# Kernel optimization log

Hardware: AMD Instinct MI355X
Metric: run time of the kernel (lower is better)

## Reference

```python
import jax, jax.numpy as jnp
import numpy as np

EMB = 768  # SentenceT5 embedding dim; MLP input is 2*EMB


def setup_inputs() -> dict:
    key = jax.random.key(0)
    ks = jax.random.split(key, 9)
    B, S, D = 32, 32, 64
    num_doc = jax.random.randint(ks[0], (B,), 8, D + 1, dtype=jnp.int32)
    num_doc = num_doc.at[0].set(D)  # ensure max == padded dim (tf.reduce_max semantics)
    num_seg = jax.random.randint(ks[1], (B,), 4, S + 1, dtype=jnp.int32)
    num_seg = num_seg.at[0].set(S)
    doc_emb = jax.random.normal(ks[2], (B, D, EMB), jnp.float32)
    sum_emb = jax.random.normal(ks[3], (B, S, EMB), jnp.float32)
    # ragged .to_tensor() -> zero rows beyond per-sample length
    doc_emb = doc_emb * (jnp.arange(D)[None, :, None] < num_doc[:, None, None])
    sum_emb = sum_emb * (jnp.arange(S)[None, :, None] < num_seg[:, None, None])
    target_agg = jax.random.uniform(ks[4], (B,), jnp.float32)
    target_inst = jax.random.uniform(ks[5], (B, S), jnp.float32)
    w = lambda k, i, o: jax.random.normal(k, (i, o), jnp.float32) * 0.02
    W1 = w(ks[6], 2 * EMB, EMB)
    b1 = jnp.zeros((EMB,), jnp.float32)
    W2 = w(ks[7], EMB, EMB // 2)
    b2 = jnp.zeros((EMB // 2,), jnp.float32)
    W3 = w(ks[8], EMB // 2, 1)
    b3 = jnp.zeros((1,), jnp.float32)
    return dict(doc_emb=doc_emb, sum_emb=sum_emb, num_document_splits=num_doc,
                num_summary_segments=num_seg, target_agg_score=target_agg,
                target_instance_score=target_inst,
                W1=W1, b1=b1, W2=W2, b2=b2, W3=W3, b3=b3)


def _forward(doc_emb, sum_emb, num_doc, num_seg, W1, b1, W2, b2, W3, b3):
    B, D, E = doc_emb.shape
    S = sum_emb.shape[1]
    # concat([doc, seg]) @ W1 == doc @ W1[:E] + seg @ W1[E:]  (avoids materializing [B,S,D,2E])
    h_doc = jnp.einsum('bde,eh->bdh', doc_emb, W1[:E])   # [B,D,E]
    h_seg = jnp.einsum('bse,eh->bsh', sum_emb, W1[E:])   # [B,S,E]
    h1 = jax.nn.gelu(h_doc[:, None, :, :] + h_seg[:, :, None, :] + b1, approximate=False)  # [B,S,D,E]
    h2 = jax.nn.gelu(jnp.einsum('bsdh,hk->bsdk', h1, W2) + b2, approximate=False)          # [B,S,D,E/2]
    score = jax.nn.sigmoid(jnp.einsum('bsdk,ko->bsdo', h2, W3) + b3)[..., 0]               # [B,S,D]
    mask_d = (jnp.arange(D)[None, :] < num_doc[:, None]).astype(jnp.float32)               # [B,D]
    seg_max = jnp.max(mask_d[:, None, :] * score, axis=-1)                                 # [B,S]
    seg_w = jnp.where(num_seg > 10, 1.0, 100.0).astype(jnp.float32)                        # [B]
    pred = seg_w[:, None] * seg_max                                                        # [B,S]
    # cosine similarity prior (keras CosineSimilarity returns -cos)
    dn = doc_emb * jax.lax.rsqrt(jnp.maximum(jnp.sum(doc_emb * doc_emb, -1, keepdims=True), 1e-12))
    sn = sum_emb * jax.lax.rsqrt(jnp.maximum(jnp.sum(sum_emb * sum_emb, -1, keepdims=True), 1e-12))
    cs = -jnp.einsum('bde,bse->bsd', dn, sn)                                               # [B,S,D]
    dscos = jnp.max(mask_d[:, None, :] * (1.0 + cs) * 0.5, axis=-1)                        # [B,S]
    seg_mask = (jnp.arange(S)[None, :] < num_seg[:, None]).astype(jnp.float32)             # [B,S]
    diff = jnp.abs(dscos - pred) * seg_mask
    cos_prior = jnp.mean(jnp.sum(diff, axis=1) / num_seg.astype(jnp.float32))
    return pred, cos_prior


def reference(doc_emb, sum_emb, num_document_splits, num_summary_segments,
              target_agg_score, target_instance_score,
              W1, b1, W2, b2, W3, b3):
    B, S = target_instance_score.shape
    seg_mask = jnp.arange(S)[None, :] < num_summary_segments[:, None]
    # pad target instance scores with ones beyond per-sample length
    target_instance = jnp.where(seg_mask, target_instance_score, 1.0)
    pred, cos_prior = _forward(doc_emb, sum_emb, num_document_splits, num_summary_segments,
                               W1, b1, W2, b2, W3, b3)
    return (target_agg_score, target_instance, pred, num_summary_segments, cos_prior)
```

## Files before the change

### kernel.cpp

```cpp
#include <hip/hip_runtime.h>
#include <hip/hip_bf16.h>
#include <math.h>


typedef __bf16 bf16x8 __attribute__((ext_vector_type(8)));
typedef float f32x4 __attribute__((ext_vector_type(4)));

__device__ __forceinline__ unsigned short f2bf(float x) {
    unsigned int u = __float_as_uint(x);
    u = (u + 0x7fffu + ((u >> 16) & 1u)) >> 16;
    return (unsigned short)u;
}
__device__ __forceinline__ float exp2_fast(float x) {
    float r; asm("v_exp_f32 %0, %1" : "=v"(r) : "v"(x)); return r;
}
__device__ __forceinline__ float rcp_fast(float x) {
    float r; asm("v_rcp_f32 %0, %1" : "=v"(r) : "v"(x)); return r;
}
__device__ __forceinline__ unsigned int cvt_pk_bf16(float lo, float hi) {
    unsigned int r; asm("v_cvt_pk_bf16_f32 %0, %1, %2" : "=v"(r) : "v"(lo), "v"(hi)); return r;
}
__device__ __forceinline__ float gelu_fast(float x) {
    float t = x * fmaf(x * x, -0.10294325f, -2.3022081f);
    return x * rcp_fast(1.0f + exp2_fast(t));
}
__device__ __forceinline__ float sigmoid_fast(float x) {
    return rcp_fast(1.0f + exp2_fast(x * -1.4426950408889634f));
}
__device__ __forceinline__ float wave_sum(float v) {
    for (int o = 32; o; o >>= 1) v += __shfl_xor(v, o);
    return v;
}
__device__ __forceinline__ float wave_max(float v) {
    for (int o = 32; o; o >>= 1) v = fmaxf(v, __shfl_xor(v, o));
    return v;
}
__device__ __forceinline__ void soft_barrier() {
    __builtin_amdgcn_sched_barrier(0);
    asm volatile("s_waitcnt lgkmcnt(0)" ::: "memory");
    __builtin_amdgcn_s_barrier();
    __builtin_amdgcn_sched_barrier(0);
}
#define GLOAD_LDS16(GP, LP)                                                     \
    __builtin_amdgcn_global_load_lds(                                           \
        (const __attribute__((address_space(1))) unsigned int*)(GP),            \
        (__attribute__((address_space(3))) unsigned int*)(LP), 16, 0, 0)

__global__ __launch_bounds__(256) void prep_all(const float* __restrict__ W1,
                                                const float* __restrict__ W2,
                                                const float* __restrict__ doc,
                                                const float* __restrict__ sume,
                                                unsigned short* __restrict__ W1t,
                                                unsigned short* __restrict__ W2f,
                                                unsigned short* __restrict__ dnbf,
                                                unsigned short* __restrict__ snbf) {
    __shared__ __align__(16) char shbuf[49152];
    int id = blockIdx.x;
    int t = threadIdx.x;
    if (id < 288) {
        float (*tile)[65] = (float(*)[65])shbuf;
        int bx = id % 12, by = id / 12;
        int r0 = by * 64, c0 = bx * 64;
        #pragma unroll
        for (int p = 0; p < 16; ++p) {
            int r = p * 4 + (t >> 6), c = t & 63;
            tile[r][c] = W1[(r0 + r) * 768 + c0 + c];
        }
        __syncthreads();
        #pragma unroll
        for (int p = 0; p < 16; ++p) {
            int cc = p * 4 + (t >> 6), rr = t & 63;
            W1t[(c0 + cc) * 1536 + r0 + rr] = f2bf(tile[rr][cc]);
        }
    } else if (id < 300) {
        unsigned short* sh = (unsigned short*)shbuf;
        int kt = id - 288;
        #pragma unroll
        for (int p = 0; p < 96; ++p) {
            int u = p * 256 + t;
            int k = u / 384, n = u - k * 384;
            sh[u] = f2bf(W2[(kt * 64 + k) * 384 + n]);
        }
        __syncthreads();
        #pragma unroll
        for (int p = 0; p < 12; ++p) {
            int u = p * 256 + t;
            int lane = u & 63;
            int g = u >> 6;
            int ks = g / 24, fc = g - ks * 24;
            unsigned short tmp[8];
            #pragma unroll
            for (int j = 0; j < 8; ++j)
                tmp[j] = sh[(ks * 32 + (lane >> 4) * 8 + j) * 384 + fc * 16 + (lane & 15)];
            int ktks = kt * 2 + ks;
            *(uint4*)(W2f + ((ktks * 24 + fc) * 64 + lane) * 8) = *(uint4*)tmp;
        }
    } else {
        int row = (id - 300) * 4 + (t >> 6);
        int lane = t & 63;
        const float* p; unsigned short* dst;
        if (row < 2048) { p = doc + row * 768; dst = dnbf + row * 768; }
        else            { p = sume + (row - 2048) * 768; dst = snbf + (row - 2048) * 768; }
        const float* pp = p + lane * 12;
        float4 a0 = *(const float4*)(pp);
        float4 a1 = *(const float4*)(pp + 4);
        float4 a2 = *(const float4*)(pp + 8);
        float s = a0.x*a0.x + a0.y*a0.y + a0.z*a0.z + a0.w*a0.w
                + a1.x*a1.x + a1.y*a1.y + a1.z*a1.z + a1.w*a1.w
                + a2.x*a2.x + a2.y*a2.y + a2.z*a2.z + a2.w*a2.w;
        s = wave_sum(s);
        float r = rsqrtf(fmaxf(s, 1e-12f));
        unsigned short* dd = dst + lane * 12;
        dd[0]  = f2bf(a0.x * r); dd[1]  = f2bf(a0.y * r);
        dd[2]  = f2bf(a0.z * r); dd[3]  = f2bf(a0.w * r);
        dd[4]  = f2bf(a1.x * r); dd[5]  = f2bf(a1.y * r);
        dd[6]  = f2bf(a1.z * r); dd[7]  = f2bf(a1.w * r);
        dd[8]  = f2bf(a2.x * r); dd[9]  = f2bf(a2.y * r);
        dd[10] = f2bf(a2.z * r); dd[11] = f2bf(a2.w * r);
    }
}

__global__ __launch_bounds__(256) void gemm1(const float* __restrict__ doc,
                                             const float* __restrict__ sume,
                                             const unsigned short* __restrict__ W1t,
                                             const float* __restrict__ b1,
                                             unsigned short* __restrict__ hd,
                                             unsigned short* __restrict__ hs) {
    __shared__ __align__(16) unsigned short Asw[2][128 * 64];
    __shared__ __align__(16) unsigned short Bsw[2][64 * 64];
    int t = threadIdx.x;
    int row0 = blockIdx.y * 128, col0 = blockIdx.x * 64;
    bool is_doc = row0 < 2048;
    const float* A = is_doc ? (doc + row0 * 768) : (sume + (row0 - 2048) * 768);
    int kbase = is_doc ? 0 : 768;
    unsigned short* O = is_doc ? (hd + row0 * 768) : (hs + (row0 - 2048) * 768);

    int l = t & 63, w = t >> 6;
    int wr = w >> 1, wc = w & 1;
    int srow = t >> 3, sko = (t & 7) * 8;
    f32x4 acc[4][2];
    #pragma unroll
    for (int i = 0; i < 4; ++i)
        #pragma unroll
        for (int j = 0; j < 2; ++j) acc[i][j] = (f32x4)0.f;

    float4 fA0[4], fA1[4];
    bf16x8 bB[2];

#define G_LOAD(KT)                                                              \
    {                                                                           \
        _Pragma("unroll")                                                       \
        for (int p = 0; p < 4; ++p) {                                           \
            fA0[p] = *(const float4*)(A + (p * 32 + srow) * 768 + (KT) + sko);  \
            fA1[p] = *(const float4*)(A + (p * 32 + srow) * 768 + (KT) + sko + 4); \
        }                                                                       \
        _Pragma("unroll")                                                       \
        for (int p = 0; p < 2; ++p)                                             \
            bB[p] = *(const bf16x8*)(W1t + (col0 + p * 32 + srow) * 1536 + kbase + (KT) + sko); \
    }

#define G_STORE(BUF)                                                            \
    {                                                                           \
        char* AB = (char*)Asw[BUF];                                             \
        char* BB = (char*)Bsw[BUF];                                             \
        _Pragma("unroll")                                                       \
        for (int p = 0; p < 4; ++p) {                                           \
            uint4 v = make_uint4(cvt_pk_bf16(fA0[p].x, fA0[p].y),               \
                                 cvt_pk_bf16(fA0[p].z, fA0[p].w),               \
                                 cvt_pk_bf16(fA1[p].x, fA1[p].y),               \
                                 cvt_pk_bf16(fA1[p].z, fA1[p].w));              \
            int r = p * 32 + srow;                                              \
            int byte = (r * 128 + sko * 2) ^ ((r & 7) << 4);                    \
            *(uint4*)(AB + byte) = v;                                           \
        }                                                                       \
        _Pragma("unroll")                                                       \
        for (int p = 0; p < 2; ++p) {                                           \
            int r = p * 32 + srow;                                              \
            int byte = (r * 128 + sko * 2) ^ ((r & 7) << 4);                    \
            *(bf16x8*)(BB + byte) = bB[p];                                      \
        }                                                                       \
    }

    G_LOAD(0)
    G_STORE(0)
    G_LOAD(64)
    soft_barrier();

    #pragma unroll 1
    for (int i = 0; i < 12; ++i) {
        int cur = i & 1;
        const char* AR = (const char*)Asw[cur];
        const char* BR = (const char*)Bsw[cur];
        #pragma unroll
        for (int ks = 0; ks < 2; ++ks) {
            int koff = (ks * 32 + (l >> 4) * 8) * 2;
            bf16x8 af[4], bfr[2];
            #pragma unroll
            for (int fr = 0; fr < 4; ++fr) {
                int r = wr * 64 + fr * 16 + (l & 15);
                af[fr] = *(const bf16x8*)(AR + ((r * 128 + koff) ^ ((r & 7) << 4)));
            }
            #pragma unroll
            for (int fc = 0; fc < 2; ++fc) {
                int n = wc * 32 + fc * 16 + (l & 15);
                bfr[fc] = *(const bf16x8*)(BR + ((n * 128 + koff) ^ ((n & 7) << 4)));
            }
            #pragma unroll
            for (int fr = 0; fr < 4; ++fr)
                #pragma unroll
                for (int fc = 0; fc < 2; ++fc)
                    acc[fr][fc] = __builtin_amdgcn_mfma_f32_16x16x32_bf16(af[fr], bfr[fc], acc[fr][fc], 0, 0, 0);
        }
        if (i < 11) {
            G_STORE(cur ^ 1)
            if (i < 10) G_LOAD((i + 2) * 64)
        }
        soft_barrier();
    }
#undef G_LOAD
#undef G_STORE

    #pragma unroll
    for (int fr = 0; fr < 4; ++fr)
        #pragma unroll
        for (int fc = 0; fc < 2; ++fc) {
            int c = col0 + wc * 32 + fc * 16 + (l & 15);
            float badd = is_doc ? 0.0f : b1[c];
            #pragma unroll
            for (int j = 0; j < 4; ++j) {
                int r = wr * 64 + fr * 16 + (l >> 4) * 4 + j;
                O[r * 768 + c] = f2bf(acc[fr][fc][j] + badd);
            }
        }
}

__global__ __launch_bounds__(512, 2) void score_mfma(
    const unsigned short* __restrict__ hd, const unsigned short* __restrict__ hs,
    const unsigned short* __restrict__ W2f,
    const float* __restrict__ b2, const float* __restrict__ W3,
    const float* __restrict__ b3, const int* __restrict__ ndoc,
    const int* __restrict__ nseg, const unsigned short* __restrict__ dnbf,
    const unsigned short* __restrict__ snbf, float* __restrict__ out,
    float* __restrict__ dscos)
{
    __shared__ __align__(16) unsigned short Asw[2][8192];
    __shared__ __align__(16) unsigned short Bsw[2][12288];
    __shared__ float spart[2][256];
    __shared__ float sred[4][32];

    int t = threadIdx.x;
    int l = t & 63, w = t >> 6;

    if (blockIdx.x >= 256) {
        int b = (int)blockIdx.x - 256;
        if (w < 4) {
            const unsigned short* sb = snbf + b * 32 * 768;
            const unsigned short* db = dnbf + b * 64 * 768;
            int arow = l & 15, ak = (l >> 4) * 8;
            int d0 = w * 16;
            f32x4 acc0 = (f32x4)0.f, acc1 = (f32x4)0.f;
            #pragma unroll
            for (int k = 0; k < 768; k += 32) {
                bf16x8 a0 = *(const bf16x8*)(sb + arow * 768 + k + ak);
                bf16x8 a1 = *(const bf16x8*)(sb + (16 + arow) * 768 + k + ak);
                bf16x8 bb = *(const bf16x8*)(db + (d0 + arow) * 768 + k + ak);
                acc0 = __builtin_amdgcn_mfma_f32_16x16x32_bf16(a0, bb, acc0, 0, 0, 0);
                acc1 = __builtin_amdgcn_mfma_f32_16x16x32_bf16(a1, bb, acc1, 0, 0, 0);
            }
            int nd = ndoc[b];
            int d = d0 + (l & 15);
            float v0[4], v1[4];
            #pragma unroll
            for (int j = 0; j < 4; ++j) {
                v0[j] = (d < nd) ? (1.f - acc0[j]) * 0.5f : 0.f;
                v1[j] = (d < nd) ? (1.f - acc1[j]) * 0.5f : 0.f;
            }
            #pragma unroll
            for (int o = 1; o < 16; o <<= 1) {
                #pragma unroll
                for (int j = 0; j < 4; ++j) {
                    v0[j] = fmaxf(v0[j], __shfl_xor(v0[j], o));
                    v1[j] = fmaxf(v1[j], __shfl_xor(v1[j], o));
                }
            }
            if ((l & 15) == 0) {
                int srw = (l >> 4) * 4;
                #pragma unroll
                for (int j = 0; j < 4; ++j) {
                    sred[w][srw + j] = v0[j];
                    sred[w][16 + srw + j] = v1[j];
                }
            }
        }
        __syncthreads();
        if (t < 32)
            dscos[b * 32 + t] = fmaxf(fmaxf(sred[0][t], sred[1][t]),
                                      fmaxf(sred[2][t], sred[3][t]));
        return;
    }

    int lb = (int)(blockIdx.x & 7) * 32 + (int)(blockIdx.x >> 3);
    int b = lb >> 3, sq = lb & 7;
    int s0 = sq * 4;
    int nd = ndoc[b], ns = nseg[b];
    int wr = w >> 1, wc = w & 1;

    f32x4 acc[4][12];
    #pragma unroll
    for (int i = 0; i < 4; ++i)
        #pragma unroll
        for (int j = 0; j < 12; ++j) acc[i][j] = (f32x4)0.f;

    int g = t >> 5;
    int rloc = t & 15;
    int k8a = (t & 31) >> 4;
    int r = g * 16 + rloc;
    int d = r & 63, sl = r >> 6;
    const unsigned short* hdp = hd + (b * 64 + d) * 768 + k8a * 8;
    const unsigned short* hsp = hs + (b * 32 + s0 + sl) * 768 + k8a * 8;
    char* Ad0 = (char*)Asw[0] + g * 1024 + (t & 31) * 16;
    char* Ad1 = (char*)Asw[1] + g * 1024 + (t & 31) * 16;

    bf16x8 hd8[2], hs8[2];

#define A_LOAD(KT)                                                              \
    {                                                                           \
        hd8[0] = *(const bf16x8*)(hdp + (KT));                                  \
        hd8[1] = *(const bf16x8*)(hdp + (KT) + 16);                             \
        hs8[0] = *(const bf16x8*)(hsp + (KT));                                  \
        hs8[1] = *(const bf16x8*)(hsp + (KT) + 16);                             \
    }

#define B_STAGE(KTKS, BUF)                                                      \
    {                                                                           \
        _Pragma("unroll")                                                       \
        for (int q = 0; q < 3; ++q) {                                           \
            int fc = w * 3 + q;                                                 \
            const unsigned short* gsrc = W2f + (((KTKS) * 24 + fc) * 64 + l) * 8; \
            GLOAD_LDS16(gsrc, &Bsw[BUF][fc * 512]);                             \
        }                                                                       \
    }

#define A_STORE(DST)                                                            \
    {                                                                           \
        _Pragma("unroll")                                                       \
        for (int q = 0; q < 2; ++q) {                                           \
            const unsigned int* hu = (const unsigned int*)&hd8[q];              \
            const unsigned int* su = (const unsigned int*)&hs8[q];              \
            unsigned int au[4];                                                 \
            _Pragma("unroll")                                                   \
            for (int e = 0; e < 4; ++e) {                                       \
                float x0 = __uint_as_float(hu[e] << 16) + __uint_as_float(su[e] << 16); \
                float x1 = __uint_as_float(hu[e] & 0xffff0000u) + __uint_as_float(su[e] & 0xffff0000u); \
                au[e] = cvt_pk_bf16(gelu_fast(x0), gelu_fast(x1));              \
            }                                                                   \
            *(uint4*)((DST) + q * 512) = make_uint4(au[0], au[1], au[2], au[3]); \
        }                                                                       \
    }

    B_STAGE(0, 0)
    A_LOAD(0)
    A_STORE(Ad0)
    __syncthreads();

    #pragma unroll 1
    for (int i = 0; i < 24; ++i) {
        int cur = i & 1;
        if (i < 23) {
            B_STAGE(i + 1, cur ^ 1)
            A_LOAD((i + 1) * 32)
        }
        const char* AR = (const char*)Asw[cur];
        const char* BR = (const char*)Bsw[cur];
        __builtin_amdgcn_s_setprio(1);
        bf16x8 af[4];
        #pragma unroll
        for (int fr = 0; fr < 4; ++fr)
            af[fr] = *(const bf16x8*)(AR + (wr * 4 + fr) * 1024 + l * 16);
        #pragma unroll
        for (int i2 = 0; i2 < 12; ++i2) {
            bf16x8 bq = *(const bf16x8*)(BR + (wc * 12 + i2) * 1024 + l * 16);
            #pragma unroll
            for (int fr = 0; fr < 4; ++fr)
                acc[fr][i2] = __builtin_amdgcn_mfma_f32_16x16x32_bf16(af[fr], bq, acc[fr][i2], 0, 0, 0);
        }
        __builtin_amdgcn_s_setprio(0);
        if (i < 23) A_STORE(cur ? Ad0 : Ad1)
        __builtin_amdgcn_sched_barrier(0);
        asm volatile("s_waitcnt vmcnt(0) lgkmcnt(0)" ::: "memory");
        __builtin_amdgcn_s_barrier();
        __builtin_amdgcn_sched_barrier(0);
    }
#undef A_LOAD
#undef B_STAGE
#undef A_STORE

    float b2v[12], w3v[12];
    #pragma unroll
    for (int i2 = 0; i2 < 12; ++i2) {
        int col = wc * 192 + i2 * 16 + (l & 15);
        b2v[i2] = b2[col];
        w3v[i2] = W3[col];
    }
    #pragma unroll
    for (int fr = 0; fr < 4; ++fr) {
        #pragma unroll
        for (int j = 0; j < 4; ++j) {
            float pr = 0.f;
            #pragma unroll
            for (int i2 = 0; i2 < 12; ++i2)
                pr += gelu_fast(acc[fr][i2][j] + b2v[i2]) * w3v[i2];
            pr += __shfl_xor(pr, 1);
            pr += __shfl_xor(pr, 2);
            pr += __shfl_xor(pr, 4);
            pr += __shfl_xor(pr, 8);
            if ((l & 15) == 0)
                spart[wc][wr * 64 + fr * 16 + (l >> 4) * 4 + j] = pr;
        }
    }
    __syncthreads();
    if (t < 256) {
        int row = t;
        float v = spart[0][row] + spart[1][row] + b3[0];
        float sc = sigmoid_fast(v);
        int dd = row & 63, sl2 = row >> 6;
        float m = (dd < nd) ? sc : 0.f;
        m = wave_max(m);
        if ((t & 63) == 0) {
            float segw = (ns > 10) ? 1.f : 100.f;
            out[1056 + b * 32 + s0 + sl2] = segw * m;
        }
    }
}

__global__ __launch_bounds__(1024) void finish_k(const float* __restrict__ agg,
                                                 const float* __restrict__ tinst,
                                                 const int* __restrict__ nseg,
                                                 const float* __restrict__ dscos,
                                                 float* __restrict__ out) {
    __shared__ float red[16];
    int t = threadIdx.x, lane = t & 63, w = t >> 6;
    int b = t >> 5, s = t & 31;
    int ns = nseg[b];
    out[32 + t] = (s < ns) ? tinst[t] : 1.0f;
    if (t < 32) {
        out[t] = agg[t];
        out[2080 + t] = (float)nseg[t];
    }
    float pred = out[1056 + t];
    float v = (s < ns) ? fabsf(dscos[t] - pred) / (float)ns : 0.f;
    v = wave_sum(v);
    if (lane == 0) red[w] = v;
    __syncthreads();
    if (w == 0) {
        float x = (lane < 16) ? red[lane] : 0.f;
        x = wave_sum(x);
        if (lane == 0) out[2112] = x * (1.f / 32.f);
    }
}

extern "C" void kernel_launch(void* const* d_in, const int* in_sizes, int n_in,
                              void* d_out, int out_size, void* d_ws, size_t ws_size,
                              hipStream_t stream) {
    const float* doc   = (const float*)d_in[0];
    const float* sume  = (const float*)d_in[1];
    const int*   ndoc  = (const int*)d_in[2];
    const int*   nseg  = (const int*)d_in[3];
    const float* agg   = (const float*)d_in[4];
    const float* tinst = (const float*)d_in[5];
    const float* W1    = (const float*)d_in[6];
    const float* b1    = (const float*)d_in[7];
    const float* W2    = (const float*)d_in[8];
    const float* b2    = (const float*)d_in[9];
    const float* W3    = (const float*)d_in[10];
    const float* b3    = (const float*)d_in[11];
    float* out = (float*)d_out;
    char* ws = (char*)d_ws;

    unsigned short* hd   = (unsigned short*)(ws);
    unsigned short* hs   = (unsigned short*)(ws + 3145728);
    unsigned short* W1t  = (unsigned short*)(ws + 4718592);
    unsigned short* W2f  = (unsigned short*)(ws + 7077888);
    unsigned short* dnbf = (unsigned short*)(ws + 7667712);
    unsigned short* snbf = (unsigned short*)(ws + 10813440);
    float* dscos = (float*)(ws + 12386304);

    prep_all<<<1068, 256, 0, stream>>>(W1, W2, doc, sume, W1t, W2f, dnbf, snbf);
    gemm1<<<dim3(12, 24), 256, 0, stream>>>(doc, sume, W1t, b1, hd, hs);
    score_mfma<<<288, 512, 0, stream>>>(hd, hs, W2f, b2, W3, b3, ndoc, nseg,
                                        dnbf, snbf, out, dscos);
    finish_k<<<1, 1024, 0, stream>>>(agg, tinst, nseg, dscos, out);
}
```

Baseline: 108.3 us.

## Halve score tile rows per block, doubling grid, and move cosine blocks first

The score kernel now gives each block 2 summary segments (128 rows) instead of 4 (256 rows), so the grid grows from 288 to 544 blocks. Waves are rearranged 2x4 so each wave holds 4x6 accumulators instead of 4x12, and each thread's A-tile load per k-step drops to one vector per operand. Shared memory becomes a single 64KB buffer with aliased regions, the launch-bounds occupancy hint is dropped, and the 32 cosine-prior blocks now run first. The aim is better CU coverage and lower register pressure. The cost is that each W2 tile is reloaded by twice as many blocks, and less of every B fragment is reused per load.

```diff
diff --git a/kernel.cpp b/kernel.cpp
--- a/kernel.cpp
+++ b/kernel.cpp
@@ -234,7 +234,7 @@
         }
 }
 
-__global__ __launch_bounds__(512, 2) void score_mfma(
+__global__ __launch_bounds__(512) void score_mfma(
     const unsigned short* __restrict__ hd, const unsigned short* __restrict__ hs,
     const unsigned short* __restrict__ W2f,
     const float* __restrict__ b2, const float* __restrict__ W3,
@@ -243,16 +243,15 @@
     const unsigned short* __restrict__ snbf, float* __restrict__ out,
     float* __restrict__ dscos)
 {
-    __shared__ __align__(16) unsigned short Asw[2][8192];
-    __shared__ __align__(16) unsigned short Bsw[2][12288];
-    __shared__ float spart[2][256];
-    __shared__ float sred[4][32];
+    __shared__ __align__(16) char smem[65536];
+    float* spart = (float*)smem;
+    float* sred  = (float*)smem;
 
     int t = threadIdx.x;
     int l = t & 63, w = t >> 6;
 
-    if (blockIdx.x >= 256) {
-        int b = (int)blockIdx.x - 256;
+    if (blockIdx.x < 32) {
+        int b = (int)blockIdx.x;
         if (w < 4) {
             const unsigned short* sb = snbf + b * 32 * 768;
             const unsigned short* db = dnbf + b * 64 * 768;
@@ -287,81 +286,77 @@
                 int srw = (l >> 4) * 4;
                 #pragma unroll
                 for (int j = 0; j < 4; ++j) {
-                    sred[w][srw + j] = v0[j];
-                    sred[w][16 + srw + j] = v1[j];
+                    sred[w * 32 + srw + j] = v0[j];
+                    sred[w * 32 + 16 + srw + j] = v1[j];
                 }
             }
         }
         __syncthreads();
         if (t < 32)
-            dscos[b * 32 + t] = fmaxf(fmaxf(sred[0][t], sred[1][t]),
-                                      fmaxf(sred[2][t], sred[3][t]));
+            dscos[(int)blockIdx.x * 32 + t] = fmaxf(fmaxf(sred[t], sred[32 + t]),
+                                                    fmaxf(sred[64 + t], sred[96 + t]));
         return;
     }
 
-    int lb = (int)(blockIdx.x & 7) * 32 + (int)(blockIdx.x >> 3);
-    int b = lb >> 3, sq = lb & 7;
-    int s0 = sq * 4;
+    int sb = (int)blockIdx.x - 32;
+    int lb = (sb & 7) * 64 + (sb >> 3);
+    int b = lb >> 4, sp = lb & 15;
+    int s0 = sp * 2;
     int nd = ndoc[b], ns = nseg[b];
-    int wr = w >> 1, wc = w & 1;
-
-    f32x4 acc[4][12];
+    int wr = w >> 2, wc = w & 3;
+
+    f32x4 acc[4][6];
     #pragma unroll
     for (int i = 0; i < 4; ++i)
         #pragma unroll
-        for (int j = 0; j < 12; ++j) acc[i][j] = (f32x4)0.f;
-
-    int g = t >> 5;
-    int rloc = t & 15;
-    int k8a = (t & 31) >> 4;
-    int r = g * 16 + rloc;
+        for (int j = 0; j < 6; ++j) acc[i][j] = (f32x4)0.f;
+
+    int r = t >> 2;
+    int k8 = t & 3;
     int d = r & 63, sl = r >> 6;
-    const unsigned short* hdp = hd + (b * 64 + d) * 768 + k8a * 8;
-    const unsigned short* hsp = hs + (b * 32 + s0 + sl) * 768 + k8a * 8;
-    char* Ad0 = (char*)Asw[0] + g * 1024 + (t & 31) * 16;
-    char* Ad1 = (char*)Asw[1] + g * 1024 + (t & 31) * 16;
-
-    bf16x8 hd8[2], hs8[2];
+    const unsigned short* hdp = hd + (b * 64 + d) * 768 + k8 * 8;
+    const unsigned short* hsp = hs + (b * 32 + s0 + sl) * 768 + k8 * 8;
+    int abyte = (r >> 4) * 1024 + k8 * 256 + (r & 15) * 16;
+
+    bf16x8 hd8, hs8;
 
 #define A_LOAD(KT)                                                              \
     {                                                                           \
-        hd8[0] = *(const bf16x8*)(hdp + (KT));                                  \
-        hd8[1] = *(const bf16x8*)(hdp + (KT) + 16);                             \
-        hs8[0] = *(const bf16x8*)(hsp + (KT));                                  \
-        hs8[1] = *(const bf16x8*)(hsp + (KT) + 16);                             \
-    }
-
-#define B_STAGE(KTKS, BUF)                                                      \
+        hd8 = *(const bf16x8*)(hdp + (KT));                                     \
+        hs8 = *(const bf16x8*)(hsp + (KT));                                     \
+    }
+
+#define B_STAGE(KC, BUF)                                                        \
     {                                                                           \
         _Pragma("unroll")                                                       \
         for (int q = 0; q < 3; ++q) {                                           \
             int fc = w * 3 + q;                                                 \
-            const unsigned short* gsrc = W2f + (((KTKS) * 24 + fc) * 64 + l) * 8; \
-            GLOAD_LDS16(gsrc, &Bsw[BUF][fc * 512]);                             \
+            const unsigned short* gsrc = W2f + (((KC) * 24 + fc) * 64 + l) * 8; \
+            GLOAD_LDS16(gsrc, smem + 16384 + (BUF) * 24576 + fc * 1024);        \
         }                                                                       \
     }
 
-#define A_STORE(DST)                                                            \
+#define A_STORE(BUF)                                                            \
     {                                                                           \
-        _Pragma("unroll")                                                       \
-        for (int q = 0; q < 2; ++q) {                                           \
-            const unsigned int* hu = (const unsigned int*)&hd8[q];              \
-            const unsigned int* su = (const unsigned int*)&hs8[q];              \
-            unsigned int au[4];                                                 \
-            _Pragma("unroll")                                                   \
-            for (int e = 0; e < 4; ++e) {                                       \
-                float x0 = __uint_as_float(hu[e] << 16) + __uint_as_float(su[e] << 16); \
-                float x1 = __uint_as_float(hu[e] & 0xffff0000u) + __uint_as_float(su[e] & 0xffff0000u); \
-                au[e] = cvt_pk_bf16(gelu_fast(x0), gelu_fast(x1));              \
-            }                                                                   \
-            *(uint4*)((DST) + q * 512) = make_uint4(au[0], au[1], au[2], au[3]); \
+        const unsigned int* hu = (const unsigned int*)&hd8;                     \
+        const unsigned int* su = (const unsigned int*)&hs8;                     \
+        unsigned int au[4];                                                     \
+        _Pragma("unroll")                                                       \
+        for (int e = 0; e < 4; ++e) {                                           \
+            float x0 = __uint_as_float(hu[e] << 16) + __uint_as_float(su[e] << 16); \
+            float x1 = __uint_as_float(hu[e] & 0xffff0000u) + __uint_as_float(su[e] & 0xffff0000u); \
+            au[e] = cvt_pk_bf16(gelu_fast(x0), gelu_fast(x1));                  \
         }                                                                       \
+        *(uint4*)(smem + (BUF) * 8192 + abyte) = make_uint4(au[0], au[1], au[2], au[3]); \
     }
 
     B_STAGE(0, 0)
     A_LOAD(0)
-    A_STORE(Ad0)
-    __syncthreads();
+    A_STORE(0)
+    __builtin_amdgcn_sched_barrier(0);
+    asm volatile("s_waitcnt vmcnt(0) lgkmcnt(0)" ::: "memory");
+    __builtin_amdgcn_s_barrier();
+    __builtin_amdgcn_sched_barrier(0);
 
     #pragma unroll 1
     for (int i = 0; i < 24; ++i) {
@@ -370,22 +365,22 @@
             B_STAGE(i + 1, cur ^ 1)
             A_LOAD((i + 1) * 32)
         }
-        const char* AR = (const char*)Asw[cur];
-        const char* BR = (const char*)Bsw[cur];
+        const char* AR = (const char*)smem + cur * 8192;
+        const char* BR = (const char*)smem + 16384 + cur * 24576;
         __builtin_amdgcn_s_setprio(1);
         bf16x8 af[4];
         #pragma unroll
         for (int fr = 0; fr < 4; ++fr)
             af[fr] = *(const bf16x8*)(AR + (wr * 4 + fr) * 1024 + l * 16);
         #pragma unroll
-        for (int i2 = 0; i2 < 12; ++i2) {
-            bf16x8 bq = *(const bf16x8*)(BR + (wc * 12 + i2) * 1024 + l * 16);
+        for (int i2 = 0; i2 < 6; ++i2) {
+            bf16x8 bq = *(const bf16x8*)(BR + (wc * 6 + i2) * 1024 + l * 16);
             #pragma unroll
             for (int fr = 0; fr < 4; ++fr)
                 acc[fr][i2] = __builtin_amdgcn_mfma_f32_16x16x32_bf16(af[fr], bq, acc[fr][i2], 0, 0, 0);
         }
         __builtin_amdgcn_s_setprio(0);
-        if (i < 23) A_STORE(cur ? Ad0 : Ad1)
+        if (i < 23) A_STORE(cur ^ 1)
         __builtin_amdgcn_sched_barrier(0);
         asm volatile("s_waitcnt vmcnt(0) lgkmcnt(0)" ::: "memory");
         __builtin_amdgcn_s_barrier();
@@ -395,33 +390,34 @@
 #undef B_STAGE
 #undef A_STORE
 
-    float b2v[12], w3v[12];
+    float b2v[6], w3v[6];
     #pragma unroll
-    for (int i2 = 0; i2 < 12; ++i2) {
-        int col = wc * 192 + i2 * 16 + (l & 15);
+    for (int i2 = 0; i2 < 6; ++i2) {
+        int col = wc * 96 + i2 * 16 + (l & 15);
         b2v[i2] = b2[col];
         w3v[i2] = W3[col];
     }
+    __syncthreads();
     #pragma unroll
     for (int fr = 0; fr < 4; ++fr) {
         #pragma unroll
         for (int j = 0; j < 4; ++j) {
             float pr = 0.f;
             #pragma unroll
-            for (int i2 = 0; i2 < 12; ++i2)
+            for (int i2 = 0; i2 < 6; ++i2)
                 pr += gelu_fast(acc[fr][i2][j] + b2v[i2]) * w3v[i2];
             pr += __shfl_xor(pr, 1);
             pr += __shfl_xor(pr, 2);
             pr += __shfl_xor(pr, 4);
             pr += __shfl_xor(pr, 8);
             if ((l & 15) == 0)
-                spart[wc][wr * 64 + fr * 16 + (l >> 4) * 4 + j] = pr;
+                spart[wc * 128 + wr * 64 + fr * 16 + (l >> 4) * 4 + j] = pr;
         }
     }
     __syncthreads();
-    if (t < 256) {
+    if (t < 128) {
         int row = t;
-        float v = spart[0][row] + spart[1][row] + b3[0];
+        float v = spart[row] + spart[128 + row] + spart[256 + row] + spart[384 + row] + b3[0];
         float sc = sigmoid_fast(v);
         int dd = row & 63, sl2 = row >> 6;
         float m = (dd < nd) ? sc : 0.f;
@@ -487,7 +483,7 @@
 
     prep_all<<<1068, 256, 0, stream>>>(W1, W2, doc, sume, W1t, W2f, dnbf, snbf);
     gemm1<<<dim3(12, 24), 256, 0, stream>>>(doc, sume, W1t, b1, hd, hs);
-    score_mfma<<<288, 512, 0, stream>>>(hd, hs, W2f, b2, W3, b3, ndoc, nseg,
+    score_mfma<<<544, 512, 0, stream>>>(hd, hs, W2f, b2, W3, b3, ndoc, nseg,
                                         dnbf, snbf, out, dscos);
     finish_k<<<1, 1024, 0, stream>>>(agg, tinst, nseg, dscos, out);
 }
```

New measurement: 103.3 us. 4.6% less time.
